# Optimization experiments

Hardware: AMD Instinct MI355X
Metric: run time of the kernel (lower is better)

## Reference

```python
import jax, jax.numpy as jnp
import numpy as np

H, D = 4, 128          # num_heads, per-head out dim (= hidden_feats)
IN = 256               # input feature dim for both node types
N_HOST, N_FLOW = 100000, 100000
E1, E2 = 200000, 200000  # edges for host->flow ('h2f') and flow->host ('f2h')
LN_EPS = 1e-5
SLOPE = 0.2            # GATConv default LeakyReLU negative_slope


def setup_inputs() -> dict:
    key = jax.random.key(0)
    ks = jax.random.split(key, 16)
    nrm = lambda k, s, sc=0.05: jax.random.normal(k, s, jnp.float32) * sc
    return {
        'feat_host': jax.random.normal(ks[0], (N_HOST, IN), jnp.float32),
        'feat_flow': jax.random.normal(ks[1], (N_FLOW, IN), jnp.float32),
        # GATConv params for rel h2f (src=host, dst=flow)
        'W1': nrm(ks[2], (IN, H * D)), 'al1': nrm(ks[3], (H, D)), 'ar1': nrm(ks[4], (H, D)), 'b1': jnp.zeros((H * D,), jnp.float32),
        # GATConv params for rel f2h (src=flow, dst=host)
        'W2': nrm(ks[5], (IN, H * D)), 'al2': nrm(ks[6], (H, D)), 'ar2': nrm(ks[7], (H, D)), 'b2': jnp.zeros((H * D,), jnp.float32),
        # residual projections (in_feats 256 != hidden 128)
        'projW_host': nrm(ks[8], (IN, D)), 'projb_host': jnp.zeros((D,), jnp.float32),
        'projW_flow': nrm(ks[9], (IN, D)), 'projb_flow': jnp.zeros((D,), jnp.float32),
        # LayerNorm params
        'g_host': jnp.ones((D,), jnp.float32), 'be_host': jnp.zeros((D,), jnp.float32),
        'g_flow': jnp.ones((D,), jnp.float32), 'be_flow': jnp.zeros((D,), jnp.float32),
        # edge lists
        'e1_src': jax.random.randint(ks[10], (E1,), 0, N_HOST, jnp.int32),
        'e1_dst': jax.random.randint(ks[11], (E1,), 0, N_FLOW, jnp.int32),
        'e2_src': jax.random.randint(ks[12], (E2,), 0, N_FLOW, jnp.int32),
        'e2_dst': jax.random.randint(ks[13], (E2,), 0, N_HOST, jnp.int32),
    }


def _gat_rel(h_src, h_dst, src, dst, W, al, ar, b, n_dst):
    """DGL GATConv (shared fc, residual=False, bias=True, eval-mode dropout)."""
    fs = (h_src @ W).reshape(-1, H, D)                     # [Ns,H,D]
    fd = (h_dst @ W).reshape(-1, H, D)                     # [Nd,H,D]
    el = jnp.sum(fs * al, axis=-1)                         # [Ns,H]
    er = jnp.sum(fd * ar, axis=-1)                         # [Nd,H]
    e = jax.nn.leaky_relu(el[src] + er[dst], SLOPE)        # [E,H]
    # edge softmax over incoming edges of each dst node (per head), max-stabilized
    m = jax.ops.segment_max(e, dst, num_segments=n_dst)    # [Nd,H]
    ee = jnp.exp(e - m[dst])
    s = jax.ops.segment_sum(ee, dst, num_segments=n_dst)   # [Nd,H]
    a = ee / s[dst]                                        # [E,H]
    msg = a[:, :, None] * fs[src]                          # [E,H,D]
    rst = jax.ops.segment_sum(msg, dst, num_segments=n_dst)  # [Nd,H,D]
    return rst + b.reshape(H, D)


def _tail(agg, feat, pW, pb, g, be):
    """mean over heads -> residual(projected) -> LayerNorm -> GELU (dropout=eval)."""
    h = agg.mean(axis=1)                                   # [N,D]
    c = h + (feat @ pW + pb)
    mu = c.mean(axis=-1, keepdims=True)
    var = ((c - mu) ** 2).mean(axis=-1, keepdims=True)
    y = (c - mu) / jnp.sqrt(var + LN_EPS) * g + be
    return jax.nn.gelu(y, approximate=False)


def reference(feat_host, feat_flow, W1, al1, ar1, b1, W2, al2, ar2, b2,
              projW_host, projb_host, projW_flow, projb_flow,
              g_host, be_host, g_flow, be_flow,
              e1_src, e1_dst, e2_src, e2_dst):
    flow_agg = _gat_rel(feat_host, feat_flow, e1_src, e1_dst, W1, al1, ar1, b1, N_FLOW)
    host_agg = _gat_rel(feat_flow, feat_host, e2_src, e2_dst, W2, al2, ar2, b2, N_HOST)
    host_out = _tail(host_agg, feat_host, projW_host, projb_host, g_host, be_host)
    flow_out = _tail(flow_agg, feat_flow, projW_flow, projb_flow, g_flow, be_flow)
    return host_out, flow_out
```

## Files before the change

kernel.cpp:

```cpp
#include <hip/hip_runtime.h>
#include <math.h>

#define NN 100000
#define EE 200000
#define HH 4
#define DD 128
#define HD 512
#define KIN 256
#define LN_EPS 1e-5f
#define SLOPE 0.2f
#define NB_SCAN 98

#define CSW(a) ((a) ^ (((a) >> 5) & 31))

typedef short bf16x8 __attribute__((ext_vector_type(8)));
typedef unsigned short u16x4 __attribute__((ext_vector_type(4)));
typedef float f32x4 __attribute__((ext_vector_type(4)));

typedef __attribute__((address_space(3))) unsigned int lds_uint;
typedef const __attribute__((address_space(1))) unsigned int glb_uint;

static __device__ __forceinline__ void gload_lds16(const void* g, void* l) {
  __builtin_amdgcn_global_load_lds((glb_uint*)g, (lds_uint*)l, 16, 0, 0);
}

static __device__ __forceinline__ unsigned short f2bf(float x) {
  unsigned int u = __float_as_uint(x);
  u += 0x7fffu + ((u >> 16) & 1u);
  return (unsigned short)(u >> 16);
}
static __device__ __forceinline__ float bf_lo(unsigned int u) {
  return __uint_as_float(u << 16);
}
static __device__ __forceinline__ float bf_hi(unsigned int u) {
  return __uint_as_float(u & 0xffff0000u);
}

static __device__ __forceinline__ float erf_fast(float x) {
  float ax = fabsf(x);
  float t = __builtin_amdgcn_rcpf(fmaf(0.3275911f, ax, 1.0f));
  float p = fmaf(1.061405429f, t, -1.453152027f);
  p = fmaf(p, t, 1.421413741f);
  p = fmaf(p, t, -0.284496736f);
  p = fmaf(p, t, 0.254829592f);
  p = p * t;
  float r = 1.0f - p * __expf(-ax * ax);
  return copysignf(r, x);
}
static __device__ __forceinline__ float gelu_fast(float y) {
  return 0.5f * y * (1.0f + erf_fast(y * 0.70710678118f));
}

__global__ __launch_bounds__(256) void convw(
    const float* __restrict__ W1, const float* __restrict__ W2,
    const float* __restrict__ pWh, const float* __restrict__ pWf,
    short* __restrict__ W1t, short* __restrict__ W2t,
    short* __restrict__ pWht, short* __restrict__ pWft) {
  int idx = blockIdx.x * 256 + threadIdx.x;
  if (idx < 512 * 256) {
    int n = idx >> 8, k = idx & 255;
    W1t[idx] = (short)f2bf(W1[(size_t)k * HD + n]);
    W2t[idx] = (short)f2bf(W2[(size_t)k * HD + n]);
  }
  if (idx < 128 * 256) {
    int n = idx >> 8, k = idx & 255;
    pWht[idx] = (short)f2bf(pWh[(size_t)k * DD + n]);
    pWft[idx] = (short)f2bf(pWf[(size_t)k * DD + n]);
  }
}

__global__ __launch_bounds__(256) void make_c(
    const float* __restrict__ W1, const float* __restrict__ al1, const float* __restrict__ ar1,
    const float* __restrict__ W2, const float* __restrict__ al2, const float* __restrict__ ar2,
    float* __restrict__ Cout, short* __restrict__ CtH, short* __restrict__ CtF) {
  int which = blockIdx.y;
  const float* W = (which < 2) ? W1 : W2;
  const float* a = (which == 0) ? al1 : (which == 1) ? ar1 : (which == 2) ? al2 : ar2;
  int k = threadIdx.x;
  float* C = Cout + (size_t)which * 1024;
#pragma unroll
  for (int h = 0; h < HH; h++) {
    float s = 0.f;
    for (int d = 0; d < DD; d++) s = fmaf(W[(size_t)k * HD + h * DD + d], a[h * DD + d], s);
    C[k * HH + h] = s;
    short b = (short)f2bf(s);
    if (which == 0)      CtH[h * KIN + k] = b;
    else if (which == 3) CtH[(4 + h) * KIN + k] = b;
    else if (which == 1) CtF[h * KIN + k] = b;
    else                 CtF[(4 + h) * KIN + k] = b;
  }
  if (which == 0) {
#pragma unroll
    for (int j = 0; j < 8; j++) CtH[(8 + j) * KIN + k] = 0;
  } else if (which == 1) {
#pragma unroll
    for (int j = 0; j < 8; j++) CtF[(8 + j) * KIN + k] = 0;
  }
}

__global__ __launch_bounds__(256) void make_bm(
    const float* __restrict__ b1, const float* __restrict__ pbf,
    const float* __restrict__ b2, const float* __restrict__ pbh,
    float* __restrict__ bm) {
  int d = threadIdx.x;
  if (d < 128) {
    bm[d] = 0.25f * (b1[d] + b1[128 + d] + b1[256 + d] + b1[384 + d]) + pbf[d];
  } else {
    int dd = d - 128;
    bm[d] = 0.25f * (b2[dd] + b2[128 + dd] + b2[256 + dd] + b2[384 + dd]) + pbh[dd];
  }
}

__global__ __launch_bounds__(256) void prep_mfma(
    const float* __restrict__ XH, const float* __restrict__ XF,
    const short* __restrict__ CtH, const short* __restrict__ CtF,
    short* __restrict__ XbH, short* __restrict__ XbF,
    float* __restrict__ o1H, float* __restrict__ o2H,
    float* __restrict__ o1F, float* __restrict__ o2F, int M) {
  __shared__ short Asm[64 * 256];
  __shared__ float os[64 * 8];
  int which = blockIdx.y;
  const float* X = which ? XF : XH;
  const short* Ct = which ? CtF : CtH;
  short* Xb = which ? XbF : XbH;
  float* o1 = which ? o1F : o1H;
  float* o2 = which ? o2F : o2H;
  int t = threadIdx.x, lane = t & 63, wid = t >> 6;
  int row0 = blockIdx.x * 64;

  {
    int rsub = t >> 5;
    int c16 = t & 31;
#pragma unroll
    for (int i = 0; i < 8; i++) {
      int r_loc = i * 8 + rsub;
      int grow = row0 + r_loc; if (grow > M - 1) grow = M - 1;
      const float* xp = X + (size_t)grow * KIN + c16 * 8;
      float4 v0 = *(const float4*)xp;
      float4 v1 = *(const float4*)(xp + 4);
      bf16x8 af;
      af[0] = (short)f2bf(v0.x); af[1] = (short)f2bf(v0.y);
      af[2] = (short)f2bf(v0.z); af[3] = (short)f2bf(v0.w);
      af[4] = (short)f2bf(v1.x); af[5] = (short)f2bf(v1.y);
      af[6] = (short)f2bf(v1.z); af[7] = (short)f2bf(v1.w);
      *(bf16x8*)(Xb + (size_t)grow * KIN + c16 * 8) = af;
      int swc = c16 ^ (r_loc & 7);
      *(bf16x8*)((char*)Asm + r_loc * 512 + swc * 16) = af;
    }
  }
  int lr = lane & 15, lk = lane >> 4;
  bf16x8 bfrag[8];
#pragma unroll
  for (int kc = 0; kc < 8; kc++)
    bfrag[kc] = *(const bf16x8*)(Ct + lr * KIN + kc * 32 + lk * 8);
  __syncthreads();

  {
    int lrow = wid * 16 + lr;
    f32x4 acc = (f32x4){0.f, 0.f, 0.f, 0.f};
#pragma unroll
    for (int kc = 0; kc < 8; kc++) {
      int chunk = (lk + kc * 4) ^ (lrow & 7);
      bf16x8 af = *(bf16x8*)((char*)Asm + lrow * 512 + chunk * 16);
      acc = __builtin_amdgcn_mfma_f32_16x16x32_bf16(af, bfrag[kc], acc, 0, 0, 0);
    }
    if (lr < 8) {
#pragma unroll
      for (int r = 0; r < 4; r++)
        os[(wid * 16 + lk * 4 + r) * 8 + lr] = acc[r];
    }
  }
  __syncthreads();

  if (t < 64) {
    int row = row0 + t;
    if (row < M)
      *(float4*)(o1 + (size_t)row * HH) =
          make_float4(os[t * 8 + 0], os[t * 8 + 1], os[t * 8 + 2], os[t * 8 + 3]);
  } else if (t < 128) {
    int j = t - 64;
    int row = row0 + j;
    if (row < M)
      *(float4*)(o2 + (size_t)row * HH) =
          make_float4(os[j * 8 + 4], os[j * 8 + 5], os[j * 8 + 6], os[j * 8 + 7]);
  }
}

__global__ __launch_bounds__(256) void skinny8(
    const float* __restrict__ X, const float* __restrict__ C1, const float* __restrict__ C2,
    float* __restrict__ o1, float* __restrict__ o2, int M) {
  __shared__ float Cs[KIN * 8];
  int tid = threadIdx.x;
  for (int i = tid; i < KIN * 4; i += 256) {
    int k = i >> 2, h = i & 3;
    Cs[CSW(k * 8 + h)] = C1[i];
    Cs[CSW(k * 8 + 4 + h)] = C2[i];
  }
  __syncthreads();
  int wave = tid >> 6, lane = tid & 63;
  int n = blockIdx.x * 4 + wave;
  if (n >= M) return;
  float4 xv = ((const float4*)(X + (size_t)n * KIN))[lane];
  float xs[4] = {xv.x, xv.y, xv.z, xv.w};
  float acc[8] = {0.f, 0.f, 0.f, 0.f, 0.f, 0.f, 0.f, 0.f};
#pragma unroll
  for (int j = 0; j < 4; j++) {
    int k = lane * 4 + j;
#pragma unroll
    for (int t = 0; t < 8; t++) acc[t] = fmaf(xs[j], Cs[CSW(k * 8 + t)], acc[t]);
  }
#pragma unroll
  for (int off = 32; off >= 1; off >>= 1)
#pragma unroll
    for (int t = 0; t < 8; t++) acc[t] += __shfl_xor(acc[t], off);
  if (lane == 0) {
#pragma unroll
    for (int h = 0; h < HH; h++) {
      o1[(size_t)n * HH + h] = acc[h];
      o2[(size_t)n * HH + h] = acc[4 + h];
    }
  }
}

__global__ __launch_bounds__(256) void hist2(
    const int* __restrict__ d1, const int* __restrict__ d2,
    int* __restrict__ c1, int* __restrict__ c2) {
  int gid = blockIdx.x * 256 + threadIdx.x;
  if (gid < EE) atomicAdd(&c1[d1[gid]], 1);
  else if (gid < 2 * EE) atomicAdd(&c2[d2[gid - EE]], 1);
}

__global__ __launch_bounds__(256) void scan_chunk(
    const int* __restrict__ c1, const int* __restrict__ c2,
    int* __restrict__ rp1, int* __restrict__ rp2, int* __restrict__ bsum) {
  int rel = blockIdx.y;
  const int* counts = rel ? c2 : c1;
  int* rowptr = rel ? rp2 : rp1;
  int* bs = bsum + rel * 128;
  __shared__ int sd[256];
  int tid = threadIdx.x;
  int base = blockIdx.x * 1024 + tid * 4;
  int c[4];
#pragma unroll
  for (int j = 0; j < 4; j++) c[j] = (base + j < NN) ? counts[base + j] : 0;
  int tot = c[0] + c[1] + c[2] + c[3];
  sd[tid] = tot; __syncthreads();
  for (int o = 1; o < 256; o <<= 1) {
    int v = (tid >= o) ? sd[tid - o] : 0;
    __syncthreads();
    sd[tid] += v;
    __syncthreads();
  }
  int excl = sd[tid] - tot;
  int run = excl;
#pragma unroll
  for (int j = 0; j < 4; j++) {
    if (base + j < NN) rowptr[base + j] = run;
    run += c[j];
  }
  if (tid == 255) bs[blockIdx.x] = sd[255];
}

__global__ __launch_bounds__(128) void scan_bsum(int* __restrict__ bsum) {
  int rel = blockIdx.y;
  int* bs = bsum + rel * 128;
  __shared__ int sd[128];
  int tid = threadIdx.x;
  int v = (tid < NB_SCAN) ? bs[tid] : 0;
  sd[tid] = v; __syncthreads();
  for (int o = 1; o < 128; o <<= 1) {
    int t = (tid >= o) ? sd[tid - o] : 0;
    __syncthreads();
    sd[tid] += t;
    __syncthreads();
  }
  bs[tid] = sd[tid] - v;
}

__global__ __launch_bounds__(256) void addoff2(
    int* __restrict__ rp1, int* __restrict__ rp2,
    int* __restrict__ cur1, int* __restrict__ cur2,
    const int* __restrict__ bsum) {
  int rel = blockIdx.y;
  int* rowptr = rel ? rp2 : rp1;
  int* cur = rel ? cur2 : cur1;
  const int* bs = bsum + rel * 128;
  int i = blockIdx.x * 256 + threadIdx.x;
  if (i < NN) {
    int r = rowptr[i] + bs[i >> 10];
    rowptr[i] = r;
    cur[i] = r;
  }
  if (i == 0) rowptr[NN] = EE;
}

__global__ __launch_bounds__(256) void fill_s(
    const int* __restrict__ e1s, const int* __restrict__ e1d,
    const int* __restrict__ e2s, const int* __restrict__ e2d,
    const float* __restrict__ el1, const float* __restrict__ er1,
    const float* __restrict__ el2, const float* __restrict__ er2,
    int* __restrict__ cur1, int* __restrict__ cur2,
    int* __restrict__ adj1, int* __restrict__ adj2,
    float* __restrict__ wexp1, float* __restrict__ wexp2) {
  int gid = blockIdx.x * 256 + threadIdx.x;
  int rel = (gid >= EE);
  if (gid >= 2 * EE) return;
  int e = rel ? gid - EE : gid;
  const int* srcp = rel ? e2s : e1s;
  const int* dstp = rel ? e2d : e1d;
  const float* el = rel ? el2 : el1;
  const float* er = rel ? er2 : er1;
  int* cur = rel ? cur2 : cur1;
  int* adj = rel ? adj2 : adj1;
  float* wexp = rel ? wexp2 : wexp1;
  int si = srcp[e], di = dstp[e];
  int p = atomicAdd(&cur[di], 1);
  adj[p] = si;
  float4 l = *(const float4*)(el + (size_t)si * HH);
  float4 r = *(const float4*)(er + (size_t)di * HH);
  float v0 = l.x + r.x, v1 = l.y + r.y, v2 = l.z + r.z, v3 = l.w + r.w;
  v0 = v0 > 0.f ? v0 : SLOPE * v0; v1 = v1 > 0.f ? v1 : SLOPE * v1;
  v2 = v2 > 0.f ? v2 : SLOPE * v2; v3 = v3 > 0.f ? v3 : SLOPE * v3;
  *(float4*)(wexp + (size_t)p * HH) =
      make_float4(__expf(v0), __expf(v1), __expf(v2), __expf(v3));
}

template <int ABF>
__global__ __launch_bounds__(256) void mfma_gemm(
    const void* __restrict__ Av, const short* __restrict__ Wt,
    void* __restrict__ Cout, int ldC, int M, int write_bf, int ncol) {
  __shared__ short As[128 * 64];
  __shared__ short Bs[128 * 64];
  int nwg = gridDim.x;
  int q = nwg >> 3, r = nwg & 7;
  int xcd = blockIdx.x & 7, seq = blockIdx.x >> 3;
  int lid = (xcd < r) ? (xcd * (q + 1) + seq) : (r * (q + 1) + (xcd - r) * q + seq);
  int row0 = (lid / ncol) * 128;
  int col0 = (lid % ncol) * 128;

  int tid = threadIdx.x;
  int lane = tid & 63, wid = tid >> 6;
  int wm = wid >> 1, wn = wid & 1;

  f32x4 acc[4][4];
#pragma unroll
  for (int i = 0; i < 4; i++)
#pragma unroll
    for (int j = 0; j < 4; j++) acc[i][j] = (f32x4){0.f, 0.f, 0.f, 0.f};

  int am = tid >> 1;
  int akh = (tid & 1) * 32;
  bool arow_ok = (row0 + am) < M;

  for (int k0 = 0; k0 < KIN; k0 += 64) {
    __syncthreads();
    if (ABF) {
      int rr8 = lane >> 3;
      int bby = (lane & 7) * 16;
#pragma unroll
      for (int c2 = 0; c2 < 4; c2++) {
        int rr = wid * 32 + c2 * 8 + rr8;
        int rg = row0 + rr; if (rg > M - 1) rg = M - 1;
        int sb = bby ^ ((rr & 7) << 4);
        gload_lds16((const char*)Av + (size_t)rg * (KIN * 2) + k0 * 2 + sb,
                    (char*)As + wid * 4096 + c2 * 1024);
      }
#pragma unroll
      for (int c2 = 0; c2 < 4; c2++) {
        int rr = wid * 32 + c2 * 8 + rr8;
        int sb = bby ^ ((rr & 7) << 4);
        gload_lds16((const char*)Wt + (size_t)(col0 + rr) * (KIN * 2) + k0 * 2 + sb,
                    (char*)Bs + wid * 4096 + c2 * 1024);
      }
    } else {
      const float* xp = (const float*)Av + (size_t)(row0 + am) * KIN + k0 + akh;
#pragma unroll
      for (int c = 0; c < 4; c++) {
        float4 v0, v1;
        if (arow_ok) {
          v0 = *(const float4*)(xp + c * 8);
          v1 = *(const float4*)(xp + c * 8 + 4);
        } else {
          v0 = make_float4(0.f, 0.f, 0.f, 0.f);
          v1 = v0;
        }
        bf16x8 pk;
        pk[0] = (short)f2bf(v0.x); pk[1] = (short)f2bf(v0.y);
        pk[2] = (short)f2bf(v0.z); pk[3] = (short)f2bf(v0.w);
        pk[4] = (short)f2bf(v1.x); pk[5] = (short)f2bf(v1.y);
        pk[6] = (short)f2bf(v1.z); pk[7] = (short)f2bf(v1.w);
        int kc = akh + c * 8;
        int ad = (am * 128 + kc * 2) ^ ((am & 7) << 4);
        *(bf16x8*)((char*)As + ad) = pk;
      }
      int bn = tid >> 1;
      int bkh = (tid & 1) * 32;
      const short* wp = Wt + (size_t)(col0 + bn) * KIN + k0 + bkh;
#pragma unroll
      for (int c = 0; c < 4; c++) {
        bf16x8 pv = *(const bf16x8*)(wp + c * 8);
        int kc = bkh + c * 8;
        int bd = (bn * 128 + kc * 2) ^ ((bn & 7) << 4);
        *(bf16x8*)((char*)Bs + bd) = pv;
      }
    }
    __syncthreads();
#pragma unroll
    for (int ks = 0; ks < 2; ks++) {
      int kb = ks * 32 + (lane >> 4) * 8;
      bf16x8 af[4], bfv[4];
#pragma unroll
      for (int mf = 0; mf < 4; mf++) {
        int rr = wm * 64 + mf * 16 + (lane & 15);
        int ad = (rr * 128 + kb * 2) ^ ((rr & 7) << 4);
        af[mf] = *(bf16x8*)((char*)As + ad);
      }
#pragma unroll
      for (int nf = 0; nf < 4; nf++) {
        int cc = wn * 64 + nf * 16 + (lane & 15);
        int bd = (cc * 128 + kb * 2) ^ ((cc & 7) << 4);
        bfv[nf] = *(bf16x8*)((char*)Bs + bd);
      }
#pragma unroll
      for (int mf = 0; mf < 4; mf++)
#pragma unroll
        for (int nf = 0; nf < 4; nf++)
          acc[mf][nf] = __builtin_amdgcn_mfma_f32_16x16x32_bf16(af[mf], bfv[nf], acc[mf][nf], 0, 0, 0);
    }
  }
  int lr = lane >> 4, lc = lane & 15;
#pragma unroll
  for (int mf = 0; mf < 4; mf++) {
#pragma unroll
    for (int r4 = 0; r4 < 4; r4++) {
      int row = row0 + wm * 64 + mf * 16 + lr * 4 + r4;
      if (row < M) {
#pragma unroll
        for (int nf = 0; nf < 4; nf++) {
          int col = col0 + wn * 64 + nf * 16 + lc;
          float v = acc[mf][nf][r4];
          if (write_bf) ((unsigned short*)Cout)[(size_t)row * ldC + col] = f2bf(v);
          else ((float*)Cout)[(size_t)row * ldC + col] = v;
        }
      }
    }
  }
}

__global__ __launch_bounds__(256) void agg2(
    const int* __restrict__ rowptr, const int* __restrict__ adj,
    const float* __restrict__ wexp,
    const unsigned short* __restrict__ fsb,
    const float* __restrict__ bm,
    const float* __restrict__ g, const float* __restrict__ be,
    float* __restrict__ out, int M) {
  int wave = threadIdx.x >> 6, lane = threadIdx.x & 63;
  int n = blockIdx.x * 4 + wave;
  if (n >= M) return;
  int beg = rowptr[n], end = rowptr[n + 1];
  int lh = lane >> 4, lc = lane & 15;
  float sh = 0.f;
  float m[8] = {0.f, 0.f, 0.f, 0.f, 0.f, 0.f, 0.f, 0.f};
  for (int t = beg; t < end; t++) {
    int si = adj[t];
    float wh = wexp[(size_t)t * HH + lh];
    sh += wh;
    uint4 u = *(const uint4*)(fsb + (size_t)si * HD + lane * 8);
    m[0] = fmaf(wh, bf_lo(u.x), m[0]); m[1] = fmaf(wh, bf_hi(u.x), m[1]);
    m[2] = fmaf(wh, bf_lo(u.y), m[2]); m[3] = fmaf(wh, bf_hi(u.y), m[3]);
    m[4] = fmaf(wh, bf_lo(u.z), m[4]); m[5] = fmaf(wh, bf_hi(u.z), m[5]);
    m[6] = fmaf(wh, bf_lo(u.w), m[6]); m[7] = fmaf(wh, bf_hi(u.w), m[7]);
  }
  float rsh = sh > 0.f ? 0.25f / sh : 0.f;
#pragma unroll
  for (int j = 0; j < 8; j++) m[j] *= rsh;
#pragma unroll
  for (int j = 0; j < 8; j++) {
    m[j] += __shfl_xor(m[j], 16);
    m[j] += __shfl_xor(m[j], 32);
  }
  const float4* bmp = (const float4*)(bm + lc * 8);
  float4 b0 = bmp[0], b1 = bmp[1];
  const float4* orow = (const float4*)(out + (size_t)n * DD + lc * 8);
  float4 p0 = orow[0], p1 = orow[1];
  float c[8];
  c[0] = m[0] + b0.x + p0.x; c[1] = m[1] + b0.y + p0.y;
  c[2] = m[2] + b0.z + p0.z; c[3] = m[3] + b0.w + p0.w;
  c[4] = m[4] + b1.x + p1.x; c[5] = m[5] + b1.y + p1.y;
  c[6] = m[6] + b1.z + p1.z; c[7] = m[7] + b1.w + p1.w;
  float ss = c[0] + c[1] + c[2] + c[3] + c[4] + c[5] + c[6] + c[7];
  ss += __shfl_xor(ss, 1); ss += __shfl_xor(ss, 2);
  ss += __shfl_xor(ss, 4); ss += __shfl_xor(ss, 8);
  float mu = ss * (1.f / 128.f);
  float vv = 0.f;
#pragma unroll
  for (int j = 0; j < 8; j++) { float d = c[j] - mu; vv = fmaf(d, d, vv); }
  vv += __shfl_xor(vv, 1); vv += __shfl_xor(vv, 2);
  vv += __shfl_xor(vv, 4); vv += __shfl_xor(vv, 8);
  float inv = rsqrtf(vv * (1.f / 128.f) + LN_EPS);
  const float4* gp = (const float4*)(g + lc * 8);
  const float4* bep = (const float4*)(be + lc * 8);
  float4 g0 = gp[0], g1 = gp[1];
  float4 e0 = bep[0], e1 = bep[1];
  float gv[8] = {g0.x, g0.y, g0.z, g0.w, g1.x, g1.y, g1.z, g1.w};
  float ev[8] = {e0.x, e0.y, e0.z, e0.w, e1.x, e1.y, e1.z, e1.w};
  float o[8];
#pragma unroll
  for (int j = 0; j < 8; j++) {
    float y = (c[j] - mu) * inv * gv[j] + ev[j];
    o[j] = gelu_fast(y);
  }
  if (lane < 16) {
    float4* op = (float4*)(out + (size_t)n * DD + lane * 8);
    op[0] = make_float4(o[0], o[1], o[2], o[3]);
    op[1] = make_float4(o[4], o[5], o[6], o[7]);
  }
}

extern "C" void kernel_launch(void* const* d_in, const int* in_sizes, int n_in,
                              void* d_out, int out_size, void* d_ws, size_t ws_size,
                              hipStream_t stream) {
  const float* feat_host = (const float*)d_in[0];
  const float* feat_flow = (const float*)d_in[1];
  const float* W1  = (const float*)d_in[2];
  const float* al1 = (const float*)d_in[3];
  const float* ar1 = (const float*)d_in[4];
  const float* b1  = (const float*)d_in[5];
  const float* W2  = (const float*)d_in[6];
  const float* al2 = (const float*)d_in[7];
  const float* ar2 = (const float*)d_in[8];
  const float* b2  = (const float*)d_in[9];
  const float* pWh = (const float*)d_in[10];
  const float* pbh = (const float*)d_in[11];
  const float* pWf = (const float*)d_in[12];
  const float* pbf = (const float*)d_in[13];
  const float* gh  = (const float*)d_in[14];
  const float* beh = (const float*)d_in[15];
  const float* gf  = (const float*)d_in[16];
  const float* bef = (const float*)d_in[17];
  const int* e1s = (const int*)d_in[18];
  const int* e1d = (const int*)d_in[19];
  const int* e2s = (const int*)d_in[20];
  const int* e2d = (const int*)d_in[21];

  float* out = (float*)d_out;
  float* host_out = out;
  float* flow_out = out + (size_t)NN * DD;

  float* ws = (float*)d_ws;
  size_t off = 0;
  unsigned short* fsb = (unsigned short*)(ws + off); off += (size_t)NN * 256;
  short* W1t  = (short*)(ws + off); off += (512 * 256) / 2;
  short* W2t  = (short*)(ws + off); off += (512 * 256) / 2;
  short* pWht = (short*)(ws + off); off += (128 * 256) / 2;
  short* pWft = (short*)(ws + off); off += (128 * 256) / 2;
  float* el1b = ws + off; off += (size_t)NN * HH;
  float* er1b = ws + off; off += (size_t)NN * HH;
  float* el2b = ws + off; off += (size_t)NN * HH;
  float* er2b = ws + off; off += (size_t)NN * HH;
  float* Cbuf = ws + off; off += 4096;
  short* CtH  = (short*)(ws + off); off += 2048;
  short* CtF  = (short*)(ws + off); off += 2048;
  float* bm   = ws + off; off += 256;
  float* wexp1 = ws + off; off += (size_t)EE * HH;
  float* wexp2 = ws + off; off += (size_t)EE * HH;
  int* rp1  = (int*)(ws + off);
  int* rp2  = rp1 + (NN + 1);
  int* adj1 = rp2 + (NN + 1);
  int* adj2 = adj1 + EE;
  int* bsum = adj2 + EE;
  int* cur1 = bsum + 256;
  int* cur2 = cur1 + NN;
  off += (size_t)(2 * (NN + 1) + 2 * EE + 256 + 2 * NN + 4);
  size_t base_bytes = (off + 1024) * sizeof(float);
  size_t featb_bytes = (size_t)NN * KIN * 2 * 2;
  bool use_featb = ws_size >= base_bytes + featb_bytes;
  short* fhb = nullptr;
  short* ffb = nullptr;
  if (use_featb) {
    fhb = (short*)(ws + off); off += (size_t)NN * KIN / 2;
    ffb = (short*)(ws + off); off += (size_t)NN * KIN / 2;
  }

  dim3 blk(256);
  int gx = (NN + 127) / 128;
  int pm_g = (NN + 63) / 64;
  int sk_g = (NN + 3) / 4;
  int ag_g = (NN + 3) / 4;
  int ee2_g = (2 * EE + 255) / 256;
  int nn_g = (NN + 255) / 256;

  convw<<<512, blk, 0, stream>>>(W1, W2, pWh, pWf, W1t, W2t, pWht, pWft);
  make_c<<<dim3(1, 4), blk, 0, stream>>>(W1, al1, ar1, W2, al2, ar2, Cbuf, CtH, CtF);
  make_bm<<<1, blk, 0, stream>>>(b1, pbf, b2, pbh, bm);
  if (use_featb) {
    prep_mfma<<<dim3(pm_g, 2), blk, 0, stream>>>(
        feat_host, feat_flow, CtH, CtF, fhb, ffb,
        el1b, er2b, er1b, el2b, NN);
  } else {
    skinny8<<<sk_g, blk, 0, stream>>>(feat_host, Cbuf + 0,    Cbuf + 3072, el1b, er2b, NN);
    skinny8<<<sk_g, blk, 0, stream>>>(feat_flow, Cbuf + 1024, Cbuf + 2048, er1b, el2b, NN);
  }

  hipMemsetAsync(cur1, 0, (size_t)2 * NN * sizeof(int), stream);
  hist2<<<ee2_g, blk, 0, stream>>>(e1d, e2d, cur1, cur2);
  scan_chunk<<<dim3(NB_SCAN, 2), blk, 0, stream>>>(cur1, cur2, rp1, rp2, bsum);
  scan_bsum<<<dim3(1, 2), 128, 0, stream>>>(bsum);
  addoff2<<<dim3(nn_g, 2), blk, 0, stream>>>(rp1, rp2, cur1, cur2, bsum);
  fill_s<<<ee2_g, blk, 0, stream>>>(e1s, e1d, e2s, e2d, el1b, er1b, el2b, er2b,
                                    cur1, cur2, adj1, adj2, wexp1, wexp2);

  if (use_featb) {
    mfma_gemm<1><<<gx, blk, 0, stream>>>(ffb, pWft, flow_out, DD, NN, 0, 1);
    mfma_gemm<1><<<gx * 4, blk, 0, stream>>>(fhb, W1t, fsb, HD, NN, 1, 4);
  } else {
    mfma_gemm<0><<<gx, blk, 0, stream>>>(feat_flow, pWft, flow_out, DD, NN, 0, 1);
    mfma_gemm<0><<<gx * 4, blk, 0, stream>>>(feat_host, W1t, fsb, HD, NN, 1, 4);
  }
  agg2<<<ag_g, blk, 0, stream>>>(rp1, adj1, wexp1, fsb, bm, gf, bef, flow_out, NN);

  if (use_featb) {
    mfma_gemm<1><<<gx, blk, 0, stream>>>(fhb, pWht, host_out, DD, NN, 0, 1);
    mfma_gemm<1><<<gx * 4, blk, 0, stream>>>(ffb, W2t, fsb, HD, NN, 1, 4);
  } else {
    mfma_gemm<0><<<gx, blk, 0, stream>>>(feat_host, pWht, host_out, DD, NN, 0, 1);
    mfma_gemm<0><<<gx * 4, blk, 0, stream>>>(feat_flow, W2t, fsb, HD, NN, 1, 4);
  }
  agg2<<<ag_g, blk, 0, stream>>>(rp2, adj2, wexp2, fsb, bm + 128, gh, beh, host_out, NN);
}
```

Before: 455.4 us.

## Compute attention weights inside aggregation and stage prep input via LDS DMA

The edge-weight computation (leaky-relu plus exp of el[src]+er[dst]) moves out of fill_s and into agg2. This removes the wexp scratch buffers and their scattered writes and reads. In exchange agg2 does a gathered el load and an exp per edge per lane. Separately, prep_mfma now processes 32 rows per block and loads the fp32 input into LDS with global_load_lds before converting it to bf16, so only two waves issue MFMAs.

```diff
diff --git a/kernel.cpp b/kernel.cpp
--- a/kernel.cpp
+++ b/kernel.cpp
@@ -117,8 +117,9 @@
     short* __restrict__ XbH, short* __restrict__ XbF,
     float* __restrict__ o1H, float* __restrict__ o2H,
     float* __restrict__ o1F, float* __restrict__ o2F, int M) {
-  __shared__ short Asm[64 * 256];
-  __shared__ float os[64 * 8];
+  __shared__ float f32s[32 * 256];
+  __shared__ short Asm[32 * 256];
+  __shared__ float os[32 * 8];
   int which = blockIdx.y;
   const float* X = which ? XF : XH;
   const short* Ct = which ? CtF : CtH;
@@ -126,26 +127,34 @@
   float* o1 = which ? o1F : o1H;
   float* o2 = which ? o2F : o2H;
   int t = threadIdx.x, lane = t & 63, wid = t >> 6;
-  int row0 = blockIdx.x * 64;
+  int row0 = blockIdx.x * 32;
+
+#pragma unroll
+  for (int c = 0; c < 8; c++) {
+    int r_loc = wid * 8 + c;
+    int grow = row0 + r_loc; if (grow > M - 1) grow = M - 1;
+    gload_lds16(X + (size_t)grow * KIN + lane * 4,
+                (char*)f32s + r_loc * 1024);
+  }
+  __syncthreads();
 
   {
-    int rsub = t >> 5;
-    int c16 = t & 31;
-#pragma unroll
-    for (int i = 0; i < 8; i++) {
-      int r_loc = i * 8 + rsub;
-      int grow = row0 + r_loc; if (grow > M - 1) grow = M - 1;
-      const float* xp = X + (size_t)grow * KIN + c16 * 8;
-      float4 v0 = *(const float4*)xp;
-      float4 v1 = *(const float4*)(xp + 4);
+    int r = t >> 3, j = t & 7;
+    int grow = row0 + r; if (grow > M - 1) grow = M - 1;
+#pragma unroll
+    for (int i = 0; i < 4; i++) {
+      int c16 = j + i * 8;
+      const float* fp = f32s + r * 256 + c16 * 8;
+      float4 v0 = *(const float4*)fp;
+      float4 v1 = *(const float4*)(fp + 4);
       bf16x8 af;
       af[0] = (short)f2bf(v0.x); af[1] = (short)f2bf(v0.y);
       af[2] = (short)f2bf(v0.z); af[3] = (short)f2bf(v0.w);
       af[4] = (short)f2bf(v1.x); af[5] = (short)f2bf(v1.y);
       af[6] = (short)f2bf(v1.z); af[7] = (short)f2bf(v1.w);
       *(bf16x8*)(Xb + (size_t)grow * KIN + c16 * 8) = af;
-      int swc = c16 ^ (r_loc & 7);
-      *(bf16x8*)((char*)Asm + r_loc * 512 + swc * 16) = af;
+      int swc = c16 ^ (r & 7);
+      *(bf16x8*)((char*)Asm + r * 512 + swc * 16) = af;
     }
   }
   int lr = lane & 15, lk = lane >> 4;
@@ -155,7 +164,7 @@
     bfrag[kc] = *(const bf16x8*)(Ct + lr * KIN + kc * 32 + lk * 8);
   __syncthreads();
 
-  {
+  if (wid < 2) {
     int lrow = wid * 16 + lr;
     f32x4 acc = (f32x4){0.f, 0.f, 0.f, 0.f};
 #pragma unroll
@@ -172,12 +181,12 @@
   }
   __syncthreads();
 
-  if (t < 64) {
+  if (t < 32) {
     int row = row0 + t;
     if (row < M)
       *(float4*)(o1 + (size_t)row * HH) =
           make_float4(os[t * 8 + 0], os[t * 8 + 1], os[t * 8 + 2], os[t * 8 + 3]);
-  } else if (t < 128) {
+  } else if (t >= 64 && t < 96) {
     int j = t - 64;
     int row = row0 + j;
     if (row < M)
@@ -297,32 +306,19 @@
 __global__ __launch_bounds__(256) void fill_s(
     const int* __restrict__ e1s, const int* __restrict__ e1d,
     const int* __restrict__ e2s, const int* __restrict__ e2d,
-    const float* __restrict__ el1, const float* __restrict__ er1,
-    const float* __restrict__ el2, const float* __restrict__ er2,
     int* __restrict__ cur1, int* __restrict__ cur2,
-    int* __restrict__ adj1, int* __restrict__ adj2,
-    float* __restrict__ wexp1, float* __restrict__ wexp2) {
+    int* __restrict__ adj1, int* __restrict__ adj2) {
   int gid = blockIdx.x * 256 + threadIdx.x;
+  if (gid >= 2 * EE) return;
   int rel = (gid >= EE);
-  if (gid >= 2 * EE) return;
   int e = rel ? gid - EE : gid;
   const int* srcp = rel ? e2s : e1s;
   const int* dstp = rel ? e2d : e1d;
-  const float* el = rel ? el2 : el1;
-  const float* er = rel ? er2 : er1;
   int* cur = rel ? cur2 : cur1;
   int* adj = rel ? adj2 : adj1;
-  float* wexp = rel ? wexp2 : wexp1;
   int si = srcp[e], di = dstp[e];
   int p = atomicAdd(&cur[di], 1);
   adj[p] = si;
-  float4 l = *(const float4*)(el + (size_t)si * HH);
-  float4 r = *(const float4*)(er + (size_t)di * HH);
-  float v0 = l.x + r.x, v1 = l.y + r.y, v2 = l.z + r.z, v3 = l.w + r.w;
-  v0 = v0 > 0.f ? v0 : SLOPE * v0; v1 = v1 > 0.f ? v1 : SLOPE * v1;
-  v2 = v2 > 0.f ? v2 : SLOPE * v2; v3 = v3 > 0.f ? v3 : SLOPE * v3;
-  *(float4*)(wexp + (size_t)p * HH) =
-      make_float4(__expf(v0), __expf(v1), __expf(v2), __expf(v3));
 }
 
 template <int ABF>
@@ -449,7 +445,7 @@
 
 __global__ __launch_bounds__(256) void agg2(
     const int* __restrict__ rowptr, const int* __restrict__ adj,
-    const float* __restrict__ wexp,
+    const float* __restrict__ el, const float* __restrict__ er,
     const unsigned short* __restrict__ fsb,
     const float* __restrict__ bm,
     const float* __restrict__ g, const float* __restrict__ be,
@@ -459,11 +455,14 @@
   if (n >= M) return;
   int beg = rowptr[n], end = rowptr[n + 1];
   int lh = lane >> 4, lc = lane & 15;
+  float ern = er[(size_t)n * HH + lh];
   float sh = 0.f;
   float m[8] = {0.f, 0.f, 0.f, 0.f, 0.f, 0.f, 0.f, 0.f};
   for (int t = beg; t < end; t++) {
     int si = adj[t];
-    float wh = wexp[(size_t)t * HH + lh];
+    float v = el[(size_t)si * HH + lh] + ern;
+    v = v > 0.f ? v : SLOPE * v;
+    float wh = __expf(v);
     sh += wh;
     uint4 u = *(const uint4*)(fsb + (size_t)si * HD + lane * 8);
     m[0] = fmaf(wh, bf_lo(u.x), m[0]); m[1] = fmaf(wh, bf_hi(u.x), m[1]);
@@ -562,8 +561,6 @@
   short* CtH  = (short*)(ws + off); off += 2048;
   short* CtF  = (short*)(ws + off); off += 2048;
   float* bm   = ws + off; off += 256;
-  float* wexp1 = ws + off; off += (size_t)EE * HH;
-  float* wexp2 = ws + off; off += (size_t)EE * HH;
   int* rp1  = (int*)(ws + off);
   int* rp2  = rp1 + (NN + 1);
   int* adj1 = rp2 + (NN + 1);
@@ -584,7 +581,7 @@
 
   dim3 blk(256);
   int gx = (NN + 127) / 128;
-  int pm_g = (NN + 63) / 64;
+  int pm_g = (NN + 31) / 32;
   int sk_g = (NN + 3) / 4;
   int ag_g = (NN + 3) / 4;
   int ee2_g = (2 * EE + 255) / 256;
@@ -607,8 +604,7 @@
   scan_chunk<<<dim3(NB_SCAN, 2), blk, 0, stream>>>(cur1, cur2, rp1, rp2, bsum);
   scan_bsum<<<dim3(1, 2), 128, 0, stream>>>(bsum);
   addoff2<<<dim3(nn_g, 2), blk, 0, stream>>>(rp1, rp2, cur1, cur2, bsum);
-  fill_s<<<ee2_g, blk, 0, stream>>>(e1s, e1d, e2s, e2d, el1b, er1b, el2b, er2b,
-                                    cur1, cur2, adj1, adj2, wexp1, wexp2);
+  fill_s<<<ee2_g, blk, 0, stream>>>(e1s, e1d, e2s, e2d, cur1, cur2, adj1, adj2);
 
   if (use_featb) {
     mfma_gemm<1><<<gx, blk, 0, stream>>>(ffb, pWft, flow_out, DD, NN, 0, 1);
@@ -617,7 +613,7 @@
     mfma_gemm<0><<<gx, blk, 0, stream>>>(feat_flow, pWft, flow_out, DD, NN, 0, 1);
     mfma_gemm<0><<<gx * 4, blk, 0, stream>>>(feat_host, W1t, fsb, HD, NN, 1, 4);
   }
-  agg2<<<ag_g, blk, 0, stream>>>(rp1, adj1, wexp1, fsb, bm, gf, bef, flow_out, NN);
+  agg2<<<ag_g, blk, 0, stream>>>(rp1, adj1, el1b, er1b, fsb, bm, gf, bef, flow_out, NN);
 
   if (use_featb) {
     mfma_gemm<1><<<gx, blk, 0, stream>>>(fhb, pWht, host_out, DD, NN, 0, 1);
@@ -626,5 +622,5 @@
     mfma_gemm<0><<<gx, blk, 0, stream>>>(feat_host, pWht, host_out, DD, NN, 0, 1);
     mfma_gemm<0><<<gx * 4, blk, 0, stream>>>(feat_flow, W2t, fsb, HD, NN, 1, 4);
   }
-  agg2<<<ag_g, blk, 0, stream>>>(rp2, adj2, wexp2, fsb, bm + 128, gh, beh, host_out, NN);
-}
+  agg2<<<ag_g, blk, 0, stream>>>(rp2, adj2, el2b, er2b, fsb, bm + 128, gh, beh, host_out, NN);
+}
```

Result: no change. 451.6 us, median of 2 (-0.8%).
